# Kernel optimization log

Measured on AMD Instinct MI355X. Metric: run time of the kernel, lower is better.

## Reference

```python
import jax, jax.numpy as jnp
import numpy as np

# ---- dims (mirror reconstructed HybridSignToTextModel) ----
INPUT_SIZE = 256
CONV_CH = 512
ENC_HID = 512          # per-direction encoder GRU hidden
ENC_OUT = 2 * ENC_HID  # bidirectional concat = 1024
DEC_LAYERS = 2
DEC_HID = 512
EMB = 512
VOCAB = 8000
ATTN = 512
MAX_DEC = 50
SOS, EOS, PAD = 1, 2, 0


def _gru_cell(x, h, Wih, Whh, bih, bhh):
    # torch GRUCell math. x:(B,I) h:(B,H) Wih:(3H,I) Whh:(3H,H)
    gi = x @ Wih.T + bih
    gh = h @ Whh.T + bhh
    H = h.shape[-1]
    ir, iz, inn = gi[:, :H], gi[:, H:2*H], gi[:, 2*H:]
    hr, hz, hn = gh[:, :H], gh[:, H:2*H], gh[:, 2*H:]
    r = jax.nn.sigmoid(ir + hr)
    z = jax.nn.sigmoid(iz + hz)
    n = jnp.tanh(inn + r * hn)
    return (1.0 - z) * n + z * h


def _gru_layer(xs, h0, Wih, Whh, bih, bhh, reverse=False):
    # xs: (T,B,I) -> outputs (T,B,H), final h (B,H)
    def step(h, x):
        h = _gru_cell(x, h, Wih, Whh, bih, bhh)
        return h, h
    hT, ys = jax.lax.scan(step, h0, xs, reverse=reverse)
    return ys, hT


def _conv1d(x, w, b, stride):
    # x:(B,C,T) w:(O,C,K) 'same'-ish padding K//2
    k = w.shape[-1]
    y = jax.lax.conv_general_dilated(x, w, (stride,), [(k // 2, k // 2)],
                                     dimension_numbers=("NCH", "OIH", "NCH"))
    return y + b[None, :, None]


def setup_inputs() -> dict:
    key = jax.random.key(0)
    ks = iter(jax.random.split(key, 40))
    def rn(shape, s=0.05):
        return (jax.random.normal(next(ks), shape, dtype=jnp.float32) * s)
    p = {}
    p["features"] = jax.random.normal(next(ks), (32, 512, INPUT_SIZE), dtype=jnp.float32)
    # conv encoder: 2 conv1d layers, stride 2 each, ReLU
    p["conv_w1"] = rn((CONV_CH, INPUT_SIZE, 5)); p["conv_b1"] = rn((CONV_CH,))
    p["conv_w2"] = rn((CONV_CH, CONV_CH, 5)); p["conv_b2"] = rn((CONV_CH,))
    # bidirectional encoder GRU (1 layer)
    for d in ("f", "b"):
        p[f"enc_Wih_{d}"] = rn((3 * ENC_HID, CONV_CH))
        p[f"enc_Whh_{d}"] = rn((3 * ENC_HID, ENC_HID))
        p[f"enc_bih_{d}"] = rn((3 * ENC_HID,))
        p[f"enc_bhh_{d}"] = rn((3 * ENC_HID,))
    # hidden bridge: 2*ENC_HID -> DEC_LAYERS*DEC_HID
    p["bridge_W"] = rn((DEC_LAYERS * DEC_HID, 2 * ENC_HID)); p["bridge_b"] = rn((DEC_LAYERS * DEC_HID,))
    # decoder embedding
    p["emb"] = rn((VOCAB, EMB), 0.1)
    # Bahdanau attention
    p["attn_We"] = rn((ATTN, ENC_OUT)); p["attn_Wd"] = rn((ATTN, DEC_HID)); p["attn_v"] = rn((ATTN,))
    # decoder GRU: 2 layers; layer0 in = EMB+ENC_OUT, layer1 in = DEC_HID
    ins = [EMB + ENC_OUT, DEC_HID]
    for l in range(DEC_LAYERS):
        p[f"dec_Wih{l}"] = rn((3 * DEC_HID, ins[l]))
        p[f"dec_Whh{l}"] = rn((3 * DEC_HID, DEC_HID))
        p[f"dec_bih{l}"] = rn((3 * DEC_HID,))
        p[f"dec_bhh{l}"] = rn((3 * DEC_HID,))
    # output proj: DEC_HID + ENC_OUT -> VOCAB
    p["proj_W"] = rn((VOCAB, DEC_HID + ENC_OUT)); p["proj_b"] = rn((VOCAB,))
    return p


def reference(features, conv_w1, conv_b1, conv_w2, conv_b2,
              enc_Wih_f, enc_Whh_f, enc_bih_f, enc_bhh_f,
              enc_Wih_b, enc_Whh_b, enc_bih_b, enc_bhh_b,
              bridge_W, bridge_b, emb, attn_We, attn_Wd, attn_v,
              dec_Wih0, dec_Whh0, dec_bih0, dec_bhh0,
              dec_Wih1, dec_Whh1, dec_bih1, dec_bhh1,
              proj_W, proj_b):
    B = features.shape[0]
    # ---- conv encoder ----
    x = features.transpose(0, 2, 1)                 # (B,C,T)
    x = jax.nn.relu(_conv1d(x, conv_w1, conv_b1, 2))
    x = jax.nn.relu(_conv1d(x, conv_w2, conv_b2, 2))
    x = x.transpose(2, 0, 1)                        # (T',B,C)
    # ---- bidirectional GRU encoder ----
    h0 = jnp.zeros((B, ENC_HID), features.dtype)
    yf, hf = _gru_layer(x, h0, enc_Wih_f, enc_Whh_f, enc_bih_f, enc_bhh_f)
    yb, hb = _gru_layer(x, h0, enc_Wih_b, enc_Whh_b, enc_bih_b, enc_bhh_b, reverse=True)
    enc_out = jnp.concatenate([yf, yb], -1).transpose(1, 0, 2)   # (B,T',2H)
    combined = jnp.concatenate([hf, hb], -1)                      # (B,2H)
    dec_h = (combined @ bridge_W.T + bridge_b).reshape(B, DEC_LAYERS, DEC_HID).transpose(1, 0, 2)
    # precompute attention keys
    enc_proj = jnp.einsum("bte,ae->bta", enc_out, attn_We)       # (B,T',A)

    def attention(h_top):
        score = jnp.einsum("bta,a->bt", jnp.tanh(enc_proj + (h_top @ attn_Wd.T)[:, None, :]), attn_v)
        w = jax.nn.softmax(score, axis=-1)
        return jnp.einsum("bt,bte->be", w, enc_out)               # (B,2H)

    def decode_step(carry, _):
        tok, h = carry                                            # h: (L,B,H)
        e = emb[tok]                                              # (B,EMB)
        ctx = attention(h[-1])
        g0 = _gru_cell(jnp.concatenate([e, ctx], -1), h[0], dec_Wih0, dec_Whh0, dec_bih0, dec_bhh0)
        g1 = _gru_cell(g0, h[1], dec_Wih1, dec_Whh1, dec_bih1, dec_bhh1)
        logits = jnp.concatenate([g1, ctx], -1) @ proj_W.T + proj_b
        nxt = jnp.argmax(logits, -1)
        return (nxt, jnp.stack([g0, g1])), nxt

    init_tok = jnp.full((B,), SOS, dtype=jnp.int32)
    _, toks = jax.lax.scan(decode_step, (init_tok, dec_h), None, length=MAX_DEC - 1)
    decoded = jnp.concatenate([init_tok[:, None], toks.T], axis=1)  # (B,MAX_DEC)
    return decoded
```

## Files before the change

kernel.cpp:

```cpp
#include <hip/hip_runtime.h>
#include <math.h>

#define DINLINE __device__ __forceinline__

DINLINE float sigmoidf_(float x) { return 1.f / (1.f + expf(-x)); }

__device__ __align__(256) float g_ws[36200000];

__global__ void im2col1_kernel(const float* __restrict__ feat, float* __restrict__ P) {
  size_t i = (size_t)blockIdx.x * 256 + threadIdx.x;
  int col = (int)(i % 1280);
  int row = (int)(i / 1280);
  int c = col / 5, k = col - c * 5;
  int l = row & 255, b = row >> 8;
  int pos = 2 * l + k - 2;
  P[i] = (pos >= 0 && pos < 512) ? feat[((size_t)b * 512 + pos) * 256 + c] : 0.f;
}

__global__ void im2col2_kernel(const float* __restrict__ y1, float* __restrict__ P) {
  size_t i = (size_t)blockIdx.x * 256 + threadIdx.x;
  int col = (int)(i % 2560);
  int row = (int)(i / 2560);
  int c = col / 5, k = col - c * 5;
  int l = row & 127, b = row >> 7;
  int pos = 2 * l + k - 2;
  P[i] = (pos >= 0 && pos < 256) ? y1[((size_t)b * 256 + pos) * 512 + c] : 0.f;
}

__global__ __launch_bounds__(256) void sgemm128(
    const float* __restrict__ A, const float* __restrict__ B,
    const float* __restrict__ bias, float* __restrict__ C,
    int M, int N, int K, int relu) {
  __shared__ float As[8][132];
  __shared__ float Bs[8][132];
  int bm = blockIdx.y * 128, bn = blockIdx.x * 128;
  int tid = threadIdx.x;
  int tx = tid & 15, ty = tid >> 4;
  float acc[8][8];
#pragma unroll
  for (int i = 0; i < 8; ++i)
#pragma unroll
    for (int j = 0; j < 8; ++j) acc[i][j] = 0.f;
  int lr = tid >> 1;
  int lc = (tid & 1) * 4;
  const float* Arow = A + (size_t)(bm + lr) * K + lc;
  const float* Brow = B + (size_t)(bn + lr) * K + lc;
  for (int k0 = 0; k0 < K; k0 += 8) {
    float4 av = *(const float4*)(Arow + k0);
    float4 bv = *(const float4*)(Brow + k0);
    As[lc + 0][lr] = av.x; As[lc + 1][lr] = av.y; As[lc + 2][lr] = av.z; As[lc + 3][lr] = av.w;
    Bs[lc + 0][lr] = bv.x; Bs[lc + 1][lr] = bv.y; Bs[lc + 2][lr] = bv.z; Bs[lc + 3][lr] = bv.w;
    __syncthreads();
#pragma unroll
    for (int kk = 0; kk < 8; ++kk) {
      float4 a0 = *(const float4*)&As[kk][ty * 8];
      float4 a1 = *(const float4*)&As[kk][ty * 8 + 4];
      float4 b0 = *(const float4*)&Bs[kk][tx * 8];
      float4 b1 = *(const float4*)&Bs[kk][tx * 8 + 4];
      float aa[8] = {a0.x, a0.y, a0.z, a0.w, a1.x, a1.y, a1.z, a1.w};
      float bb[8] = {b0.x, b0.y, b0.z, b0.w, b1.x, b1.y, b1.z, b1.w};
#pragma unroll
      for (int i = 0; i < 8; ++i)
#pragma unroll
        for (int j = 0; j < 8; ++j) acc[i][j] += aa[i] * bb[j];
    }
    __syncthreads();
  }
#pragma unroll
  for (int i = 0; i < 8; ++i) {
    int m = bm + ty * 8 + i;
#pragma unroll
    for (int j = 0; j < 8; ++j) {
      int n = bn + tx * 8 + j;
      float v = acc[i][j] + (bias ? bias[n] : 0.f);
      if (relu) v = fmaxf(v, 0.f);
      C[(size_t)m * N + n] = v;
    }
  }
}

__global__ __launch_bounds__(128) void enc_gru_step(
    const float* __restrict__ gi_f, const float* __restrict__ gi_b,
    const float* __restrict__ Whh_f, const float* __restrict__ bhh_f,
    const float* __restrict__ Whh_b, const float* __restrict__ bhh_b,
    const float* __restrict__ h_in, float* __restrict__ h_out,
    float* __restrict__ enc_out, int s) {
  int dir = blockIdx.x >> 7;
  int j = ((blockIdx.x & 127) << 2) + (threadIdx.x >> 5);
  int b = threadIdx.x & 31;
  __shared__ float4 hs4[4096];
  const float4* hbase = (const float4*)(h_in + dir * 32 * 512);
  for (int i = threadIdx.x; i < 4096; i += 128) {
    int bb = i >> 7, kf = i & 127;
    hs4[(bb << 7) + (kf ^ (bb & 7))] = hbase[i];
  }
  __syncthreads();
  const float* gi = dir ? gi_b : gi_f;
  const float* Whh = dir ? Whh_b : Whh_f;
  const float* bhh = dir ? bhh_b : bhh_f;
  int t = dir ? (127 - s) : s;
  const float4* wr = (const float4*)(Whh + (size_t)j * 512);
  const float4* wz = (const float4*)(Whh + (size_t)(512 + j) * 512);
  const float4* wn = (const float4*)(Whh + (size_t)(1024 + j) * 512);
  const float4* hrow = hs4 + b * 128;
  int sw = b & 7;
  float sr = 0.f, sz = 0.f, sn = 0.f;
#pragma unroll 4
  for (int kf = 0; kf < 128; ++kf) {
    float4 hv = hrow[kf ^ sw];
    float4 r4 = wr[kf];
    float4 z4 = wz[kf];
    float4 n4 = wn[kf];
    sr += hv.x * r4.x + hv.y * r4.y + hv.z * r4.z + hv.w * r4.w;
    sz += hv.x * z4.x + hv.y * z4.y + hv.z * z4.z + hv.w * z4.w;
    sn += hv.x * n4.x + hv.y * n4.y + hv.z * n4.z + hv.w * n4.w;
  }
  const float* g = gi + ((size_t)b * 128 + t) * 1536;
  float r = sigmoidf_(g[j] + sr + bhh[j]);
  float z = sigmoidf_(g[512 + j] + sz + bhh[512 + j]);
  float n = tanhf(g[1024 + j] + r * (sn + bhh[1024 + j]));
  float4 hj4 = hrow[(j >> 2) ^ sw];
  float hj = ((const float*)&hj4)[j & 3];
  float hnew = (1.f - z) * n + z * hj;
  h_out[dir * 32 * 512 + b * 512 + j] = hnew;
  enc_out[((size_t)b * 128 + t) * 1024 + dir * 512 + j] = hnew;
}

__global__ __launch_bounds__(256) void dec_gru_fused(
    const float* __restrict__ A1, const int* __restrict__ tokidx, int len1,
    const float* __restrict__ A2, int len2,
    const float* __restrict__ Wih, const float* __restrict__ bih,
    const float* __restrict__ Whh, const float* __restrict__ bhh,
    const float* __restrict__ h_in, float* __restrict__ h_out,
    unsigned long long* __restrict__ keys_zero) {
  __shared__ float4 buf[4096];
  int tid = threadIdx.x;
  int b = tid & 31, j = (blockIdx.x << 3) + (tid >> 5);
  if (keys_zero && blockIdx.x == 0 && tid < 32) keys_zero[tid] = 0ULL;
  int Kin = len1 + len2;
  const float4* wir = (const float4*)(Wih + (size_t)j * Kin);
  const float4* wiz = (const float4*)(Wih + (size_t)(512 + j) * Kin);
  const float4* win = (const float4*)(Wih + (size_t)(1024 + j) * Kin);
  int K4 = Kin >> 2, len1_4 = len1 >> 2;
  float gr = 0.f, gz = 0.f, gn = 0.f;
  int sw5 = b & 31;
  for (int k0 = 0; k0 < K4; k0 += 32) {
    __syncthreads();
    for (int idx = tid; idx < 1024; idx += 256) {
      int bb = idx >> 5, kf = idx & 31;
      int gk = k0 + kf;
      float4 v;
      if (gk < len1_4) {
        const float* src = tokidx ? (A1 + (size_t)tokidx[bb] * len1) : (A1 + (size_t)bb * len1);
        v = ((const float4*)src)[gk];
      } else {
        v = ((const float4*)(A2 + (size_t)bb * len2))[gk - len1_4];
      }
      buf[(bb << 5) + (kf ^ (bb & 31))] = v;
    }
    __syncthreads();
    const float4* xrow = buf + (b << 5);
    const float4* wr_ = wir + k0;
    const float4* wz_ = wiz + k0;
    const float4* wn_ = win + k0;
#pragma unroll 4
    for (int kf = 0; kf < 32; ++kf) {
      float4 xv = xrow[kf ^ sw5];
      float4 r4 = wr_[kf];
      float4 z4 = wz_[kf];
      float4 n4 = wn_[kf];
      gr += xv.x * r4.x + xv.y * r4.y + xv.z * r4.z + xv.w * r4.w;
      gz += xv.x * z4.x + xv.y * z4.y + xv.z * z4.z + xv.w * z4.w;
      gn += xv.x * n4.x + xv.y * n4.y + xv.z * n4.z + xv.w * n4.w;
    }
  }
  __syncthreads();
  const float4* hbase = (const float4*)h_in;
  for (int i = tid; i < 4096; i += 256) {
    int bb = i >> 7, kf = i & 127;
    buf[(bb << 7) + (kf ^ (bb & 7))] = hbase[i];
  }
  __syncthreads();
  const float4* whr = (const float4*)(Whh + (size_t)j * 512);
  const float4* whz = (const float4*)(Whh + (size_t)(512 + j) * 512);
  const float4* whn = (const float4*)(Whh + (size_t)(1024 + j) * 512);
  const float4* hrow = buf + (b << 7);
  int sw = b & 7;
  float sr = 0.f, sz = 0.f, sn = 0.f;
#pragma unroll 4
  for (int kf = 0; kf < 128; ++kf) {
    float4 hv = hrow[kf ^ sw];
    float4 r4 = whr[kf];
    float4 z4 = whz[kf];
    float4 n4 = whn[kf];
    sr += hv.x * r4.x + hv.y * r4.y + hv.z * r4.z + hv.w * r4.w;
    sz += hv.x * z4.x + hv.y * z4.y + hv.z * z4.z + hv.w * z4.w;
    sn += hv.x * n4.x + hv.y * n4.y + hv.z * n4.z + hv.w * n4.w;
  }
  float r = sigmoidf_(gr + bih[j] + sr + bhh[j]);
  float z = sigmoidf_(gz + bih[512 + j] + sz + bhh[512 + j]);
  float n = tanhf(gn + bih[1024 + j] + r * (sn + bhh[1024 + j]));
  float4 hj4 = hrow[(j >> 2) ^ sw];
  float hj = ((const float*)&hj4)[j & 3];
  h_out[b * 512 + j] = (1.f - z) * n + z * hj;
}

__global__ __launch_bounds__(256) void gemvB(
    const float* __restrict__ A1, const int* __restrict__ tokidx, int len1,
    const float* __restrict__ A2, int len2,
    const float* __restrict__ W, const float* __restrict__ bias,
    float* __restrict__ out0, float* __restrict__ out1, int split, int N, int K) {
  int tid = threadIdx.x;
  int s = tid & 7, nl = tid >> 3;
  int n = blockIdx.x * 32 + nl;
  __shared__ float4 xs4[32 * 32];
  float acc[32];
#pragma unroll
  for (int b = 0; b < 32; ++b) acc[b] = 0.f;
  const float4* W4 = (const float4*)(W + (size_t)n * K);
  int K4 = K >> 2;
  int len1_4 = len1 >> 2;
  for (int k0 = 0; k0 < K4; k0 += 32) {
    __syncthreads();
    for (int idx = tid; idx < 1024; idx += 256) {
      int b = idx >> 5, kf = idx & 31;
      int gk = k0 + kf;
      float4 v;
      if (gk < len1_4) {
        const float* src = tokidx ? (A1 + (size_t)tokidx[b] * len1) : (A1 + (size_t)b * len1);
        v = ((const float4*)src)[gk];
      } else {
        v = ((const float4*)(A2 + (size_t)b * len2))[gk - len1_4];
      }
      xs4[idx] = v;
    }
    __syncthreads();
    const float4* wp = W4 + k0;
#pragma unroll
    for (int j = 0; j < 4; ++j) {
      float4 wv = wp[j * 8 + s];
      const float4* xp = xs4 + j * 8 + s;
#pragma unroll
      for (int b = 0; b < 32; ++b) {
        float4 xv = xp[b * 32];
        acc[b] += wv.x * xv.x + wv.y * xv.y + wv.z * xv.z + wv.w * xv.w;
      }
    }
  }
#pragma unroll
  for (int b = 0; b < 32; ++b) {
    float v = acc[b];
    v += __shfl_xor(v, 1);
    v += __shfl_xor(v, 2);
    v += __shfl_xor(v, 4);
    acc[b] = v;
  }
  if (s == 0) {
    float bv = bias ? bias[n] : 0.f;
#pragma unroll
    for (int b = 0; b < 32; ++b) {
      float val = acc[b] + bv;
      if (n < split) out0[(size_t)b * split + n] = val;
      else out1[(size_t)b * (N - split) + (n - split)] = val;
    }
  }
}

__global__ __launch_bounds__(256) void proj_argmax_kernel(
    const float* __restrict__ A1, int len1,
    const float* __restrict__ A2, int len2,
    const float* __restrict__ W, const float* __restrict__ bias,
    unsigned long long* __restrict__ keys) {
  int tid = threadIdx.x;
  int s = tid & 7, nl = tid >> 3;
  int n = blockIdx.x * 32 + nl;
  __shared__ float4 xs4[32 * 32];
  __shared__ unsigned long long ksh[32][33];
  float acc[32];
#pragma unroll
  for (int b = 0; b < 32; ++b) acc[b] = 0.f;
  int K = len1 + len2;
  const float4* W4 = (const float4*)(W + (size_t)n * K);
  int K4 = K >> 2;
  int len1_4 = len1 >> 2;
  for (int k0 = 0; k0 < K4; k0 += 32) {
    __syncthreads();
    for (int idx = tid; idx < 1024; idx += 256) {
      int b = idx >> 5, kf = idx & 31;
      int gk = k0 + kf;
      float4 v;
      if (gk < len1_4) v = ((const float4*)(A1 + (size_t)b * len1))[gk];
      else v = ((const float4*)(A2 + (size_t)b * len2))[gk - len1_4];
      xs4[idx] = v;
    }
    __syncthreads();
    const float4* wp = W4 + k0;
#pragma unroll
    for (int j = 0; j < 4; ++j) {
      float4 wv = wp[j * 8 + s];
      const float4* xp = xs4 + j * 8 + s;
#pragma unroll
      for (int b = 0; b < 32; ++b) {
        float4 xv = xp[b * 32];
        acc[b] += wv.x * xv.x + wv.y * xv.y + wv.z * xv.z + wv.w * xv.w;
      }
    }
  }
#pragma unroll
  for (int b = 0; b < 32; ++b) {
    float v = acc[b];
    v += __shfl_xor(v, 1);
    v += __shfl_xor(v, 2);
    v += __shfl_xor(v, 4);
    acc[b] = v;
  }
  if (s == 0) {
    float bv = bias[n];
#pragma unroll
    for (int b = 0; b < 32; ++b) {
      float val = acc[b] + bv;
      unsigned u = __float_as_uint(val);
      u = (u & 0x80000000u) ? ~u : (u | 0x80000000u);
      ksh[nl][b] = ((unsigned long long)u << 32) | (unsigned long long)(0xFFFFFFFFu - (unsigned)n);
    }
  }
  __syncthreads();
  if (tid < 32) {
    unsigned long long best = 0ULL;
#pragma unroll 8
    for (int q = 0; q < 32; ++q) {
      unsigned long long v = ksh[q][tid];
      if (v > best) best = v;
    }
    atomicMax(&keys[tid], best);
  }
}

__global__ __launch_bounds__(512) void attn_fused(
    const float* __restrict__ h1,
    const float* __restrict__ Wd,
    const float* __restrict__ v,
    const float* __restrict__ enc_proj,
    const float* __restrict__ enc_out,
    float* __restrict__ ctx,
    const unsigned long long* __restrict__ keys,
    int* __restrict__ tok, int* __restrict__ decoded, int step) {
  int b = blockIdx.x;
  int tid = threadIdx.x;
  if (step > 0 && b == 0 && tid < 32) {
    unsigned long long k = keys[tid];
    int n = (int)(0xFFFFFFFFu - (unsigned)(k & 0xFFFFFFFFull));
    tok[tid] = n;
    decoded[tid * 50 + step] = n;
  }
  __shared__ float hs[512];
  __shared__ float d[512];
  __shared__ float red[512];
  __shared__ float sc[128];
  hs[tid] = h1[b * 512 + tid];
  __syncthreads();
  {
    const float* w = Wd + (size_t)tid * 512;
    float s = 0.f;
    for (int k = 0; k < 512; k += 4) {
      float4 wv = *(const float4*)&w[k];
      float4 hv = *(const float4*)&hs[k];
      s += hv.x * wv.x + hv.y * wv.y + hv.z * wv.z + hv.w * wv.w;
    }
    d[tid] = s;
  }
  __syncthreads();
  {
    int t = tid >> 2, part = tid & 3;
    const float* ep = enc_proj + ((size_t)b * 128 + t) * 512 + part * 128;
    const float* dd = d + part * 128;
    const float* vv = v + part * 128;
    float s = 0.f;
    for (int a = 0; a < 128; ++a) s += tanhf(ep[a] + dd[a]) * vv[a];
    red[tid] = s;
  }
  __syncthreads();
  if (tid < 128) sc[tid] = red[tid * 4] + red[tid * 4 + 1] + red[tid * 4 + 2] + red[tid * 4 + 3];
  __syncthreads();
  if (tid == 0) {
    float m = -1e30f;
    for (int t = 0; t < 128; ++t) m = fmaxf(m, sc[t]);
    float sum = 0.f;
    for (int t = 0; t < 128; ++t) { float e = expf(sc[t] - m); sc[t] = e; sum += e; }
    float inv = 1.f / sum;
    for (int t = 0; t < 128; ++t) sc[t] *= inv;
  }
  __syncthreads();
  for (int e = tid; e < 1024; e += 512) {
    const float* eo = enc_out + (size_t)b * 131072 + e;
    float s = 0.f;
    for (int t = 0; t < 128; ++t) s += sc[t] * eo[(size_t)t * 1024];
    ctx[b * 1024 + e] = s;
  }
}

__global__ void final_tok_kernel(const unsigned long long* __restrict__ keys,
                                 int* __restrict__ decoded) {
  int b = threadIdx.x;
  if (b >= 32) return;
  int n = (int)(0xFFFFFFFFu - (unsigned)(keys[b] & 0xFFFFFFFFull));
  decoded[b * 50 + 49] = n;
}

__global__ void init_kernel(int* __restrict__ tok, int* __restrict__ decoded) {
  int b = threadIdx.x;
  if (b >= 32) return;
  tok[b] = 1;
  decoded[b * 50] = 1;
}

__global__ void zero_kernel(float* __restrict__ p, int n) {
  int i = blockIdx.x * 256 + threadIdx.x;
  if (i < n) p[i] = 0.f;
}

extern "C" void kernel_launch(void* const* d_in, const int* in_sizes, int n_in,
                              void* d_out, int out_size, void* d_ws, size_t ws_size,
                              hipStream_t stream) {
  const float* features  = (const float*)d_in[0];
  const float* conv_w1   = (const float*)d_in[1];
  const float* conv_b1   = (const float*)d_in[2];
  const float* conv_w2   = (const float*)d_in[3];
  const float* conv_b2   = (const float*)d_in[4];
  const float* enc_Wih_f = (const float*)d_in[5];
  const float* enc_Whh_f = (const float*)d_in[6];
  const float* enc_bih_f = (const float*)d_in[7];
  const float* enc_bhh_f = (const float*)d_in[8];
  const float* enc_Wih_b = (const float*)d_in[9];
  const float* enc_Whh_b = (const float*)d_in[10];
  const float* enc_bih_b = (const float*)d_in[11];
  const float* enc_bhh_b = (const float*)d_in[12];
  const float* bridge_W  = (const float*)d_in[13];
  const float* bridge_b  = (const float*)d_in[14];
  const float* emb       = (const float*)d_in[15];
  const float* attn_We   = (const float*)d_in[16];
  const float* attn_Wd   = (const float*)d_in[17];
  const float* attn_v    = (const float*)d_in[18];
  const float* dec_Wih0  = (const float*)d_in[19];
  const float* dec_Whh0  = (const float*)d_in[20];
  const float* dec_bih0  = (const float*)d_in[21];
  const float* dec_bhh0  = (const float*)d_in[22];
  const float* dec_Wih1  = (const float*)d_in[23];
  const float* dec_Whh1  = (const float*)d_in[24];
  const float* dec_bih1  = (const float*)d_in[25];
  const float* dec_bhh1  = (const float*)d_in[26];
  const float* proj_W    = (const float*)d_in[27];
  const float* proj_b    = (const float*)d_in[28];
  int* decoded = (int*)d_out;

  float* ws = nullptr;
  hipGetSymbolAddress((void**)&ws, HIP_SYMBOL(g_ws));
  float* P       = ws;
  float* y1      = ws + 10485760;
  float* x2      = ws + 14680064;
  float* gi_f    = ws + 16777216;
  float* gi_b    = ws + 23068672;
  float* enc_out = ws + 29360128;
  float* enc_pj  = ws + 33554432;
  float* h_enc   = ws + 35651584;
  float* h0d     = ws + 35717120;
  float* h1d     = ws + 35749888;
  float* ctxb    = ws + 35782656;
  unsigned long long* keys = (unsigned long long*)(ws + 35815424);
  int*   tok     = (int*)(ws + 35815488);

  im2col1_kernel<<<40960, 256, 0, stream>>>(features, P);
  sgemm128<<<dim3(4, 64), 256, 0, stream>>>(P, conv_w1, conv_b1, y1, 8192, 512, 1280, 1);
  im2col2_kernel<<<40960, 256, 0, stream>>>(y1, P);
  sgemm128<<<dim3(4, 32), 256, 0, stream>>>(P, conv_w2, conv_b2, x2, 4096, 512, 2560, 1);

  sgemm128<<<dim3(12, 32), 256, 0, stream>>>(x2, enc_Wih_f, enc_bih_f, gi_f, 4096, 1536, 512, 0);
  sgemm128<<<dim3(12, 32), 256, 0, stream>>>(x2, enc_Wih_b, enc_bih_b, gi_b, 4096, 1536, 512, 0);

  zero_kernel<<<256, 256, 0, stream>>>(h_enc, 65536);
  for (int s = 0; s < 128; ++s) {
    enc_gru_step<<<256, 128, 0, stream>>>(gi_f, gi_b,
        enc_Whh_f, enc_bhh_f, enc_Whh_b, enc_bhh_b,
        h_enc + (s & 1) * 32768, h_enc + ((s + 1) & 1) * 32768, enc_out, s);
  }
  float* h_fin = h_enc;

  gemvB<<<32, 256, 0, stream>>>(h_fin, nullptr, 512, h_fin + 16384, 512,
      bridge_W, bridge_b, h0d, h1d, 512, 1024, 1024);

  sgemm128<<<dim3(4, 32), 256, 0, stream>>>(enc_out, attn_We, nullptr, enc_pj, 4096, 512, 1024, 0);

  init_kernel<<<1, 64, 0, stream>>>(tok, decoded);

  for (int s = 0; s < 49; ++s) {
    int cur = s & 1, nxt = (s + 1) & 1;
    attn_fused<<<32, 512, 0, stream>>>(h1d + cur * 16384, attn_Wd, attn_v,
                                       enc_pj, enc_out, ctxb, keys, tok, decoded, s);
    dec_gru_fused<<<64, 256, 0, stream>>>(emb, tok, 512, ctxb, 1024,
        dec_Wih0, dec_bih0, dec_Whh0, dec_bhh0,
        h0d + cur * 16384, h0d + nxt * 16384, nullptr);
    dec_gru_fused<<<64, 256, 0, stream>>>(h0d + nxt * 16384, nullptr, 512, nullptr, 0,
        dec_Wih1, dec_bih1, dec_Whh1, dec_bhh1,
        h1d + cur * 16384, h1d + nxt * 16384, keys);
    proj_argmax_kernel<<<250, 256, 0, stream>>>(h1d + nxt * 16384, 512, ctxb, 1024,
        proj_W, proj_b, keys);
  }
  final_tok_kernel<<<1, 32, 0, stream>>>(keys, decoded);
}
```

Measured before the change: 19.93 ms.

## Replace per-step launches with persistent encoder and decoder kernels using grid barriers

The encoder GRU now runs as one persistent kernel with one block per (direction, batch). Each block keeps its hidden state in shared memory and loops over all 128 timesteps, so the 128 launches go away. The decoder's 49 steps of attention, two GRU layers and projection-argmax are fused into a single persistent 256-block kernel that synchronizes with a software global barrier, removing about 200 launches. In exchange, every encoder block rereads the full Whh matrix each step, which may make it bandwidth-bound. The spin barrier requires all 256 blocks to be co-resident and adds atomic and fence overhead at each phase.

```diff
diff --git a/kernel.cpp b/kernel.cpp
--- a/kernel.cpp
+++ b/kernel.cpp
@@ -6,6 +6,34 @@
 DINLINE float sigmoidf_(float x) { return 1.f / (1.f + expf(-x)); }
 
 __device__ __align__(256) float g_ws[36200000];
+
+__device__ unsigned g_cnt;
+__device__ unsigned g_epoch;
+
+#define GRID_BAR()                                                     \
+  do {                                                                 \
+    __syncthreads();                                                   \
+    if (threadIdx.x == 0) {                                            \
+      __threadfence();                                                 \
+      bar_target += 1u;                                                \
+      unsigned prev_ = atomicAdd(&g_cnt, 1u);                          \
+      if (prev_ == 255u) {                                             \
+        atomicExch(&g_cnt, 0u);                                        \
+        __threadfence();                                               \
+        atomicExch(&g_epoch, bar_target);                              \
+      } else {                                                         \
+        while (atomicAdd(&g_epoch, 0u) < bar_target) {                 \
+          __builtin_amdgcn_s_sleep(2);                                 \
+        }                                                              \
+      }                                                                \
+      __threadfence();                                                 \
+    }                                                                  \
+    __syncthreads();                                                   \
+  } while (0)
+
+__global__ void reset_bar_kernel() {
+  if (threadIdx.x == 0) { g_cnt = 0u; g_epoch = 0u; }
+}
 
 __global__ void im2col1_kernel(const float* __restrict__ feat, float* __restrict__ P) {
   size_t i = (size_t)blockIdx.x * 256 + threadIdx.x;
@@ -79,130 +107,54 @@
   }
 }
 
-__global__ __launch_bounds__(128) void enc_gru_step(
+__global__ __launch_bounds__(512) void enc_persist2(
     const float* __restrict__ gi_f, const float* __restrict__ gi_b,
     const float* __restrict__ Whh_f, const float* __restrict__ bhh_f,
     const float* __restrict__ Whh_b, const float* __restrict__ bhh_b,
-    const float* __restrict__ h_in, float* __restrict__ h_out,
-    float* __restrict__ enc_out, int s) {
-  int dir = blockIdx.x >> 7;
-  int j = ((blockIdx.x & 127) << 2) + (threadIdx.x >> 5);
-  int b = threadIdx.x & 31;
-  __shared__ float4 hs4[4096];
-  const float4* hbase = (const float4*)(h_in + dir * 32 * 512);
-  for (int i = threadIdx.x; i < 4096; i += 128) {
-    int bb = i >> 7, kf = i & 127;
-    hs4[(bb << 7) + (kf ^ (bb & 7))] = hbase[i];
-  }
-  __syncthreads();
-  const float* gi = dir ? gi_b : gi_f;
+    float* __restrict__ h_fin, float* __restrict__ enc_out) {
+  __shared__ float hcur[512];
+  __shared__ float gh[1536];
+  int dir = blockIdx.x >> 5;
+  int b = blockIdx.x & 31;
+  int tid = threadIdx.x;
+  int sl = tid & 7, nl = tid >> 3;
+  const float* gi  = dir ? gi_b  : gi_f;
   const float* Whh = dir ? Whh_b : Whh_f;
   const float* bhh = dir ? bhh_b : bhh_f;
-  int t = dir ? (127 - s) : s;
-  const float4* wr = (const float4*)(Whh + (size_t)j * 512);
-  const float4* wz = (const float4*)(Whh + (size_t)(512 + j) * 512);
-  const float4* wn = (const float4*)(Whh + (size_t)(1024 + j) * 512);
-  const float4* hrow = hs4 + b * 128;
-  int sw = b & 7;
-  float sr = 0.f, sz = 0.f, sn = 0.f;
+  hcur[tid] = 0.f;
+  int j = tid;
+  float bhr = bhh[j], bhz = bhh[512 + j], bhn = bhh[1024 + j];
+  __syncthreads();
+  for (int s = 0; s < 128; ++s) {
+    int t = dir ? (127 - s) : s;
 #pragma unroll 4
-  for (int kf = 0; kf < 128; ++kf) {
-    float4 hv = hrow[kf ^ sw];
-    float4 r4 = wr[kf];
-    float4 z4 = wz[kf];
-    float4 n4 = wn[kf];
-    sr += hv.x * r4.x + hv.y * r4.y + hv.z * r4.z + hv.w * r4.w;
-    sz += hv.x * z4.x + hv.y * z4.y + hv.z * z4.z + hv.w * z4.w;
-    sn += hv.x * n4.x + hv.y * n4.y + hv.z * n4.z + hv.w * n4.w;
-  }
-  const float* g = gi + ((size_t)b * 128 + t) * 1536;
-  float r = sigmoidf_(g[j] + sr + bhh[j]);
-  float z = sigmoidf_(g[512 + j] + sz + bhh[512 + j]);
-  float n = tanhf(g[1024 + j] + r * (sn + bhh[1024 + j]));
-  float4 hj4 = hrow[(j >> 2) ^ sw];
-  float hj = ((const float*)&hj4)[j & 3];
-  float hnew = (1.f - z) * n + z * hj;
-  h_out[dir * 32 * 512 + b * 512 + j] = hnew;
-  enc_out[((size_t)b * 128 + t) * 1024 + dir * 512 + j] = hnew;
-}
-
-__global__ __launch_bounds__(256) void dec_gru_fused(
-    const float* __restrict__ A1, const int* __restrict__ tokidx, int len1,
-    const float* __restrict__ A2, int len2,
-    const float* __restrict__ Wih, const float* __restrict__ bih,
-    const float* __restrict__ Whh, const float* __restrict__ bhh,
-    const float* __restrict__ h_in, float* __restrict__ h_out,
-    unsigned long long* __restrict__ keys_zero) {
-  __shared__ float4 buf[4096];
-  int tid = threadIdx.x;
-  int b = tid & 31, j = (blockIdx.x << 3) + (tid >> 5);
-  if (keys_zero && blockIdx.x == 0 && tid < 32) keys_zero[tid] = 0ULL;
-  int Kin = len1 + len2;
-  const float4* wir = (const float4*)(Wih + (size_t)j * Kin);
-  const float4* wiz = (const float4*)(Wih + (size_t)(512 + j) * Kin);
-  const float4* win = (const float4*)(Wih + (size_t)(1024 + j) * Kin);
-  int K4 = Kin >> 2, len1_4 = len1 >> 2;
-  float gr = 0.f, gz = 0.f, gn = 0.f;
-  int sw5 = b & 31;
-  for (int k0 = 0; k0 < K4; k0 += 32) {
-    __syncthreads();
-    for (int idx = tid; idx < 1024; idx += 256) {
-      int bb = idx >> 5, kf = idx & 31;
-      int gk = k0 + kf;
-      float4 v;
-      if (gk < len1_4) {
-        const float* src = tokidx ? (A1 + (size_t)tokidx[bb] * len1) : (A1 + (size_t)bb * len1);
-        v = ((const float4*)src)[gk];
-      } else {
-        v = ((const float4*)(A2 + (size_t)bb * len2))[gk - len1_4];
-      }
-      buf[(bb << 5) + (kf ^ (bb & 31))] = v;
-    }
-    __syncthreads();
-    const float4* xrow = buf + (b << 5);
-    const float4* wr_ = wir + k0;
-    const float4* wz_ = wiz + k0;
-    const float4* wn_ = win + k0;
-#pragma unroll 4
-    for (int kf = 0; kf < 32; ++kf) {
-      float4 xv = xrow[kf ^ sw5];
-      float4 r4 = wr_[kf];
-      float4 z4 = wz_[kf];
-      float4 n4 = wn_[kf];
-      gr += xv.x * r4.x + xv.y * r4.y + xv.z * r4.z + xv.w * r4.w;
-      gz += xv.x * z4.x + xv.y * z4.y + xv.z * z4.z + xv.w * z4.w;
-      gn += xv.x * n4.x + xv.y * n4.y + xv.z * n4.z + xv.w * n4.w;
-    }
-  }
-  __syncthreads();
-  const float4* hbase = (const float4*)h_in;
-  for (int i = tid; i < 4096; i += 256) {
-    int bb = i >> 7, kf = i & 127;
-    buf[(bb << 7) + (kf ^ (bb & 7))] = hbase[i];
-  }
-  __syncthreads();
-  const float4* whr = (const float4*)(Whh + (size_t)j * 512);
-  const float4* whz = (const float4*)(Whh + (size_t)(512 + j) * 512);
-  const float4* whn = (const float4*)(Whh + (size_t)(1024 + j) * 512);
-  const float4* hrow = buf + (b << 7);
-  int sw = b & 7;
-  float sr = 0.f, sz = 0.f, sn = 0.f;
-#pragma unroll 4
-  for (int kf = 0; kf < 128; ++kf) {
-    float4 hv = hrow[kf ^ sw];
-    float4 r4 = whr[kf];
-    float4 z4 = whz[kf];
-    float4 n4 = whn[kf];
-    sr += hv.x * r4.x + hv.y * r4.y + hv.z * r4.z + hv.w * r4.w;
-    sz += hv.x * z4.x + hv.y * z4.y + hv.z * z4.z + hv.w * z4.w;
-    sn += hv.x * n4.x + hv.y * n4.y + hv.z * n4.z + hv.w * n4.w;
-  }
-  float r = sigmoidf_(gr + bih[j] + sr + bhh[j]);
-  float z = sigmoidf_(gz + bih[512 + j] + sz + bhh[512 + j]);
-  float n = tanhf(gn + bih[1024 + j] + r * (sn + bhh[1024 + j]));
-  float4 hj4 = hrow[(j >> 2) ^ sw];
-  float hj = ((const float*)&hj4)[j & 3];
-  h_out[b * 512 + j] = (1.f - z) * n + z * hj;
+    for (int pass = 0; pass < 24; ++pass) {
+      int m = pass * 64 + nl;
+      const float4* wp = (const float4*)(Whh + (size_t)m * 512);
+      float a = 0.f;
+#pragma unroll
+      for (int q = 0; q < 16; ++q) {
+        float4 wv = wp[q * 8 + sl];
+        float4 hv = *(const float4*)&hcur[(q * 8 + sl) * 4];
+        a += wv.x * hv.x + wv.y * hv.y + wv.z * hv.z + wv.w * hv.w;
+      }
+      a += __shfl_xor(a, 1);
+      a += __shfl_xor(a, 2);
+      a += __shfl_xor(a, 4);
+      if (sl == 0) gh[m] = a;
+    }
+    __syncthreads();
+    const float* g = gi + ((size_t)b * 128 + t) * 1536;
+    float r = sigmoidf_(g[j] + gh[j] + bhr);
+    float z = sigmoidf_(g[512 + j] + gh[512 + j] + bhz);
+    float n = tanhf(g[1024 + j] + r * (gh[1024 + j] + bhn));
+    float hnew = (1.f - z) * n + z * hcur[j];
+    __syncthreads();
+    hcur[j] = hnew;
+    enc_out[((size_t)b * 128 + t) * 1024 + dir * 512 + j] = hnew;
+    __syncthreads();
+  }
+  h_fin[dir * 16384 + b * 512 + j] = hcur[j];
 }
 
 __global__ __launch_bounds__(256) void gemvB(
@@ -266,145 +218,265 @@
   }
 }
 
-__global__ __launch_bounds__(256) void proj_argmax_kernel(
-    const float* __restrict__ A1, int len1,
-    const float* __restrict__ A2, int len2,
-    const float* __restrict__ W, const float* __restrict__ bias,
-    unsigned long long* __restrict__ keys) {
-  int tid = threadIdx.x;
-  int s = tid & 7, nl = tid >> 3;
-  int n = blockIdx.x * 32 + nl;
-  __shared__ float4 xs4[32 * 32];
-  __shared__ unsigned long long ksh[32][33];
-  float acc[32];
-#pragma unroll
-  for (int b = 0; b < 32; ++b) acc[b] = 0.f;
-  int K = len1 + len2;
-  const float4* W4 = (const float4*)(W + (size_t)n * K);
-  int K4 = K >> 2;
-  int len1_4 = len1 >> 2;
-  for (int k0 = 0; k0 < K4; k0 += 32) {
-    __syncthreads();
-    for (int idx = tid; idx < 1024; idx += 256) {
-      int b = idx >> 5, kf = idx & 31;
-      int gk = k0 + kf;
-      float4 v;
-      if (gk < len1_4) v = ((const float4*)(A1 + (size_t)b * len1))[gk];
-      else v = ((const float4*)(A2 + (size_t)b * len2))[gk - len1_4];
-      xs4[idx] = v;
-    }
-    __syncthreads();
-    const float4* wp = W4 + k0;
-#pragma unroll
-    for (int j = 0; j < 4; ++j) {
-      float4 wv = wp[j * 8 + s];
-      const float4* xp = xs4 + j * 8 + s;
+__global__ __launch_bounds__(256) void dec_persist(
+    const float* __restrict__ emb, const float* __restrict__ attn_Wd,
+    const float* __restrict__ attn_v,
+    const float* __restrict__ enc_pj, const float* __restrict__ enc_out,
+    const float* __restrict__ dec_Wih0, const float* __restrict__ dec_bih0,
+    const float* __restrict__ dec_Whh0, const float* __restrict__ dec_bhh0,
+    const float* __restrict__ dec_Wih1, const float* __restrict__ dec_bih1,
+    const float* __restrict__ dec_Whh1, const float* __restrict__ dec_bhh1,
+    const float* __restrict__ proj_W, const float* __restrict__ proj_b,
+    float* __restrict__ h0d, float* __restrict__ h1d,
+    float* __restrict__ ctxb, float* __restrict__ dbuf,
+    unsigned long long* __restrict__ keys, int* __restrict__ tok,
+    int* __restrict__ decoded) {
+  __shared__ float4 SB[1024];
+  __shared__ unsigned long long ksh[32 * 33];
+  __shared__ float d_s[512];
+  __shared__ float red_s[256];
+  __shared__ float sc_s[128];
+  unsigned bar_target = 0u;
+  int blk = blockIdx.x, tid = threadIdx.x;
+  int s8 = tid & 7, nl = tid >> 3;
+  int bb31 = tid & 31, jj = tid >> 5;
+
+  for (int s = 0; s < 49; ++s) {
+    int cur = s & 1, nxt = (s + 1) & 1;
+    const float* h1cur = h1d + cur * 16384;
+
+    if (blk < 16) {
+      int n = blk * 32 + nl;
+      float acc[32];
+#pragma unroll
+      for (int b = 0; b < 32; ++b) acc[b] = 0.f;
+      const float4* W4 = (const float4*)(attn_Wd + (size_t)n * 512);
+      for (int k0 = 0; k0 < 128; k0 += 32) {
+        __syncthreads();
+        for (int idx = tid; idx < 1024; idx += 256) {
+          int b = idx >> 5, kf = idx & 31;
+          SB[idx] = ((const float4*)(h1cur + (size_t)b * 512))[k0 + kf];
+        }
+        __syncthreads();
+        const float4* wp = W4 + k0;
+#pragma unroll
+        for (int j = 0; j < 4; ++j) {
+          float4 wv = wp[j * 8 + s8];
+          const float4* xp = SB + j * 8 + s8;
+#pragma unroll
+          for (int b = 0; b < 32; ++b) {
+            float4 xv = xp[b * 32];
+            acc[b] += wv.x * xv.x + wv.y * xv.y + wv.z * xv.z + wv.w * xv.w;
+          }
+        }
+      }
 #pragma unroll
       for (int b = 0; b < 32; ++b) {
-        float4 xv = xp[b * 32];
-        acc[b] += wv.x * xv.x + wv.y * xv.y + wv.z * xv.z + wv.w * xv.w;
-      }
-    }
-  }
-#pragma unroll
-  for (int b = 0; b < 32; ++b) {
-    float v = acc[b];
-    v += __shfl_xor(v, 1);
-    v += __shfl_xor(v, 2);
-    v += __shfl_xor(v, 4);
-    acc[b] = v;
-  }
-  if (s == 0) {
-    float bv = bias[n];
-#pragma unroll
-    for (int b = 0; b < 32; ++b) {
-      float val = acc[b] + bv;
-      unsigned u = __float_as_uint(val);
-      u = (u & 0x80000000u) ? ~u : (u | 0x80000000u);
-      ksh[nl][b] = ((unsigned long long)u << 32) | (unsigned long long)(0xFFFFFFFFu - (unsigned)n);
-    }
-  }
-  __syncthreads();
-  if (tid < 32) {
-    unsigned long long best = 0ULL;
+        float v = acc[b];
+        v += __shfl_xor(v, 1);
+        v += __shfl_xor(v, 2);
+        v += __shfl_xor(v, 4);
+        if (s8 == 0) dbuf[(size_t)b * 512 + n] = v;
+      }
+    } else if (blk == 16 && s > 0 && tid < 32) {
+      unsigned long long k = keys[tid];
+      int n = (int)(0xFFFFFFFFu - (unsigned)(k & 0xFFFFFFFFull));
+      tok[tid] = n;
+      decoded[tid * 50 + s] = n;
+    }
+    GRID_BAR();
+
+    if (blk < 32) {
+      int b = blk;
+      d_s[tid] = dbuf[b * 512 + tid];
+      d_s[tid + 256] = dbuf[b * 512 + tid + 256];
+      __syncthreads();
+      {
+        int t = tid >> 1, part = tid & 1;
+        const float* ep = enc_pj + ((size_t)b * 128 + t) * 512 + part * 256;
+        const float* dd = d_s + part * 256;
+        const float* vv = attn_v + part * 256;
+        float sv = 0.f;
+        for (int a = 0; a < 256; ++a) sv += tanhf(ep[a] + dd[a]) * vv[a];
+        red_s[tid] = sv;
+      }
+      __syncthreads();
+      if (tid < 128) sc_s[tid] = red_s[tid * 2] + red_s[tid * 2 + 1];
+      __syncthreads();
+      if (tid == 0) {
+        float m = -1e30f;
+        for (int t = 0; t < 128; ++t) m = fmaxf(m, sc_s[t]);
+        float sum = 0.f;
+        for (int t = 0; t < 128; ++t) { float e = expf(sc_s[t] - m); sc_s[t] = e; sum += e; }
+        float inv = 1.f / sum;
+        for (int t = 0; t < 128; ++t) sc_s[t] *= inv;
+      }
+      __syncthreads();
+      for (int e = tid; e < 1024; e += 256) {
+        const float* eo = enc_out + (size_t)b * 131072 + e;
+        float sv = 0.f;
+        for (int t = 0; t < 128; ++t) sv += sc_s[t] * eo[(size_t)t * 1024];
+        ctxb[b * 1024 + e] = sv;
+      }
+    } else if (blk == 32 && tid < 32) {
+      keys[tid] = 0ULL;
+    }
+    GRID_BAR();
+
+    for (int layer = 0; layer < 2; ++layer) {
+      if (blk < 64) {
+        const float* A1   = layer ? (h0d + nxt * 16384) : emb;
+        const int* tki    = layer ? (const int*)0 : tok;
+        int len1          = 512;
+        const float* A2   = layer ? (const float*)0 : ctxb;
+        int len2          = layer ? 0 : 1024;
+        const float* Wih  = layer ? dec_Wih1 : dec_Wih0;
+        const float* bih  = layer ? dec_bih1 : dec_bih0;
+        const float* Whh  = layer ? dec_Whh1 : dec_Whh0;
+        const float* bhh  = layer ? dec_bhh1 : dec_bhh0;
+        const float* h_in = layer ? (h1d + cur * 16384) : (h0d + cur * 16384);
+        float* h_out      = layer ? (h1d + nxt * 16384) : (h0d + nxt * 16384);
+        int b = bb31, j = (blk << 3) + jj;
+        int Kin = len1 + len2;
+        int K4 = Kin >> 2, len1_4 = len1 >> 2;
+        int sw5 = b & 31;
+        const float4* wir = (const float4*)(Wih + (size_t)j * Kin);
+        const float4* wiz = (const float4*)(Wih + (size_t)(512 + j) * Kin);
+        const float4* win = (const float4*)(Wih + (size_t)(1024 + j) * Kin);
+        float gr = 0.f, gz = 0.f, gn = 0.f;
+        for (int k0 = 0; k0 < K4; k0 += 32) {
+          __syncthreads();
+          for (int idx = tid; idx < 1024; idx += 256) {
+            int bs = idx >> 5, kf = idx & 31;
+            int gk = k0 + kf;
+            float4 v;
+            if (gk < len1_4) {
+              const float* src = tki ? (A1 + (size_t)tki[bs] * len1) : (A1 + (size_t)bs * len1);
+              v = ((const float4*)src)[gk];
+            } else {
+              v = ((const float4*)(A2 + (size_t)bs * len2))[gk - len1_4];
+            }
+            SB[(bs << 5) + (kf ^ (bs & 31))] = v;
+          }
+          __syncthreads();
+          const float4* xrow = SB + (b << 5);
+          const float4* wr_ = wir + k0;
+          const float4* wz_ = wiz + k0;
+          const float4* wn_ = win + k0;
+#pragma unroll 4
+          for (int kf = 0; kf < 32; ++kf) {
+            float4 xv = xrow[kf ^ sw5];
+            float4 r4 = wr_[kf];
+            float4 z4 = wz_[kf];
+            float4 n4 = wn_[kf];
+            gr += xv.x * r4.x + xv.y * r4.y + xv.z * r4.z + xv.w * r4.w;
+            gz += xv.x * z4.x + xv.y * z4.y + xv.z * z4.z + xv.w * z4.w;
+            gn += xv.x * n4.x + xv.y * n4.y + xv.z * n4.z + xv.w * n4.w;
+          }
+        }
+        const float4* whr = (const float4*)(Whh + (size_t)j * 512);
+        const float4* whz = (const float4*)(Whh + (size_t)(512 + j) * 512);
+        const float4* whn = (const float4*)(Whh + (size_t)(1024 + j) * 512);
+        float sr = 0.f, sz = 0.f, sn = 0.f;
+        for (int k0 = 0; k0 < 128; k0 += 32) {
+          __syncthreads();
+          for (int idx = tid; idx < 1024; idx += 256) {
+            int bs = idx >> 5, kf = idx & 31;
+            float4 v = ((const float4*)(h_in + (size_t)bs * 512))[k0 + kf];
+            SB[(bs << 5) + (kf ^ (bs & 31))] = v;
+          }
+          __syncthreads();
+          const float4* xrow = SB + (b << 5);
+          const float4* wr_ = whr + k0;
+          const float4* wz_ = whz + k0;
+          const float4* wn_ = whn + k0;
+#pragma unroll 4
+          for (int kf = 0; kf < 32; ++kf) {
+            float4 xv = xrow[kf ^ sw5];
+            float4 r4 = wr_[kf];
+            float4 z4 = wz_[kf];
+            float4 n4 = wn_[kf];
+            sr += xv.x * r4.x + xv.y * r4.y + xv.z * r4.z + xv.w * r4.w;
+            sz += xv.x * z4.x + xv.y * z4.y + xv.z * z4.z + xv.w * z4.w;
+            sn += xv.x * n4.x + xv.y * n4.y + xv.z * n4.z + xv.w * n4.w;
+          }
+        }
+        float r = sigmoidf_(gr + bih[j] + sr + bhh[j]);
+        float z = sigmoidf_(gz + bih[512 + j] + sz + bhh[512 + j]);
+        float n = tanhf(gn + bih[1024 + j] + r * (sn + bhh[1024 + j]));
+        float hj = h_in[b * 512 + j];
+        h_out[b * 512 + j] = (1.f - z) * n + z * hj;
+      }
+      GRID_BAR();
+    }
+
+    if (blk < 250) {
+      const float* h1n = h1d + nxt * 16384;
+      int n = blk * 32 + nl;
+      float acc[32];
+#pragma unroll
+      for (int b = 0; b < 32; ++b) acc[b] = 0.f;
+      const float4* W4 = (const float4*)(proj_W + (size_t)n * 1536);
+      for (int k0 = 0; k0 < 384; k0 += 32) {
+        __syncthreads();
+        for (int idx = tid; idx < 1024; idx += 256) {
+          int b = idx >> 5, kf = idx & 31;
+          int gk = k0 + kf;
+          float4 v;
+          if (gk < 128) v = ((const float4*)(h1n + (size_t)b * 512))[gk];
+          else v = ((const float4*)(ctxb + (size_t)b * 1024))[gk - 128];
+          SB[idx] = v;
+        }
+        __syncthreads();
+        const float4* wp = W4 + k0;
+#pragma unroll
+        for (int j = 0; j < 4; ++j) {
+          float4 wv = wp[j * 8 + s8];
+          const float4* xp = SB + j * 8 + s8;
+#pragma unroll
+          for (int b = 0; b < 32; ++b) {
+            float4 xv = xp[b * 32];
+            acc[b] += wv.x * xv.x + wv.y * xv.y + wv.z * xv.z + wv.w * xv.w;
+          }
+        }
+      }
+#pragma unroll
+      for (int b = 0; b < 32; ++b) {
+        float v = acc[b];
+        v += __shfl_xor(v, 1);
+        v += __shfl_xor(v, 2);
+        v += __shfl_xor(v, 4);
+        acc[b] = v;
+      }
+      if (s8 == 0) {
+        float bv = proj_b[n];
+#pragma unroll
+        for (int b = 0; b < 32; ++b) {
+          float val = acc[b] + bv;
+          unsigned u = __float_as_uint(val);
+          u = (u & 0x80000000u) ? ~u : (u | 0x80000000u);
+          ksh[nl * 33 + b] =
+              ((unsigned long long)u << 32) | (unsigned long long)(0xFFFFFFFFu - (unsigned)n);
+        }
+      }
+      __syncthreads();
+      if (tid < 32) {
+        unsigned long long best = 0ULL;
 #pragma unroll 8
-    for (int q = 0; q < 32; ++q) {
-      unsigned long long v = ksh[q][tid];
-      if (v > best) best = v;
-    }
-    atomicMax(&keys[tid], best);
-  }
-}
-
-__global__ __launch_bounds__(512) void attn_fused(
-    const float* __restrict__ h1,
-    const float* __restrict__ Wd,
-    const float* __restrict__ v,
-    const float* __restrict__ enc_proj,
-    const float* __restrict__ enc_out,
-    float* __restrict__ ctx,
-    const unsigned long long* __restrict__ keys,
-    int* __restrict__ tok, int* __restrict__ decoded, int step) {
-  int b = blockIdx.x;
-  int tid = threadIdx.x;
-  if (step > 0 && b == 0 && tid < 32) {
+        for (int q = 0; q < 32; ++q) {
+          unsigned long long v = ksh[q * 33 + tid];
+          if (v > best) best = v;
+        }
+        atomicMax(&keys[tid], best);
+      }
+      __syncthreads();
+    }
+    GRID_BAR();
+  }
+  if (blk == 0 && tid < 32) {
     unsigned long long k = keys[tid];
-    int n = (int)(0xFFFFFFFFu - (unsigned)(k & 0xFFFFFFFFull));
-    tok[tid] = n;
-    decoded[tid * 50 + step] = n;
-  }
-  __shared__ float hs[512];
-  __shared__ float d[512];
-  __shared__ float red[512];
-  __shared__ float sc[128];
-  hs[tid] = h1[b * 512 + tid];
-  __syncthreads();
-  {
-    const float* w = Wd + (size_t)tid * 512;
-    float s = 0.f;
-    for (int k = 0; k < 512; k += 4) {
-      float4 wv = *(const float4*)&w[k];
-      float4 hv = *(const float4*)&hs[k];
-      s += hv.x * wv.x + hv.y * wv.y + hv.z * wv.z + hv.w * wv.w;
-    }
-    d[tid] = s;
-  }
-  __syncthreads();
-  {
-    int t = tid >> 2, part = tid & 3;
-    const float* ep = enc_proj + ((size_t)b * 128 + t) * 512 + part * 128;
-    const float* dd = d + part * 128;
-    const float* vv = v + part * 128;
-    float s = 0.f;
-    for (int a = 0; a < 128; ++a) s += tanhf(ep[a] + dd[a]) * vv[a];
-    red[tid] = s;
-  }
-  __syncthreads();
-  if (tid < 128) sc[tid] = red[tid * 4] + red[tid * 4 + 1] + red[tid * 4 + 2] + red[tid * 4 + 3];
-  __syncthreads();
-  if (tid == 0) {
-    float m = -1e30f;
-    for (int t = 0; t < 128; ++t) m = fmaxf(m, sc[t]);
-    float sum = 0.f;
-    for (int t = 0; t < 128; ++t) { float e = expf(sc[t] - m); sc[t] = e; sum += e; }
-    float inv = 1.f / sum;
-    for (int t = 0; t < 128; ++t) sc[t] *= inv;
-  }
-  __syncthreads();
-  for (int e = tid; e < 1024; e += 512) {
-    const float* eo = enc_out + (size_t)b * 131072 + e;
-    float s = 0.f;
-    for (int t = 0; t < 128; ++t) s += sc[t] * eo[(size_t)t * 1024];
-    ctx[b * 1024 + e] = s;
-  }
-}
-
-__global__ void final_tok_kernel(const unsigned long long* __restrict__ keys,
-                                 int* __restrict__ decoded) {
-  int b = threadIdx.x;
-  if (b >= 32) return;
-  int n = (int)(0xFFFFFFFFu - (unsigned)(keys[b] & 0xFFFFFFFFull));
-  decoded[b * 50 + 49] = n;
+    decoded[tid * 50 + 49] = (int)(0xFFFFFFFFu - (unsigned)(k & 0xFFFFFFFFull));
+  }
 }
 
 __global__ void init_kernel(int* __restrict__ tok, int* __restrict__ decoded) {
@@ -412,11 +484,6 @@
   if (b >= 32) return;
   tok[b] = 1;
   decoded[b * 50] = 1;
-}
-
-__global__ void zero_kernel(float* __restrict__ p, int n) {
-  int i = blockIdx.x * 256 + threadIdx.x;
-  if (i < n) p[i] = 0.f;
 }
 
 extern "C" void kernel_launch(void* const* d_in, const int* in_sizes, int n_in,
@@ -468,6 +535,7 @@
   float* ctxb    = ws + 35782656;
   unsigned long long* keys = (unsigned long long*)(ws + 35815424);
   int*   tok     = (int*)(ws + 35815488);
+  float* dbuf    = ws + 35815520;
 
   im2col1_kernel<<<40960, 256, 0, stream>>>(features, P);
   sgemm128<<<dim3(4, 64), 256, 0, stream>>>(P, conv_w1, conv_b1, y1, 8192, 512, 1280, 1);
@@ -477,33 +545,19 @@
   sgemm128<<<dim3(12, 32), 256, 0, stream>>>(x2, enc_Wih_f, enc_bih_f, gi_f, 4096, 1536, 512, 0);
   sgemm128<<<dim3(12, 32), 256, 0, stream>>>(x2, enc_Wih_b, enc_bih_b, gi_b, 4096, 1536, 512, 0);
 
-  zero_kernel<<<256, 256, 0, stream>>>(h_enc, 65536);
-  for (int s = 0; s < 128; ++s) {
-    enc_gru_step<<<256, 128, 0, stream>>>(gi_f, gi_b,
-        enc_Whh_f, enc_bhh_f, enc_Whh_b, enc_bhh_b,
-        h_enc + (s & 1) * 32768, h_enc + ((s + 1) & 1) * 32768, enc_out, s);
-  }
-  float* h_fin = h_enc;
-
-  gemvB<<<32, 256, 0, stream>>>(h_fin, nullptr, 512, h_fin + 16384, 512,
+  enc_persist2<<<64, 512, 0, stream>>>(gi_f, gi_b,
+      enc_Whh_f, enc_bhh_f, enc_Whh_b, enc_bhh_b, h_enc, enc_out);
+
+  gemvB<<<32, 256, 0, stream>>>(h_enc, nullptr, 512, h_enc + 16384, 512,
       bridge_W, bridge_b, h0d, h1d, 512, 1024, 1024);
 
   sgemm128<<<dim3(4, 32), 256, 0, stream>>>(enc_out, attn_We, nullptr, enc_pj, 4096, 512, 1024, 0);
 
   init_kernel<<<1, 64, 0, stream>>>(tok, decoded);
-
-  for (int s = 0; s < 49; ++s) {
-    int cur = s & 1, nxt = (s + 1) & 1;
-    attn_fused<<<32, 512, 0, stream>>>(h1d + cur * 16384, attn_Wd, attn_v,
-                                       enc_pj, enc_out, ctxb, keys, tok, decoded, s);
-    dec_gru_fused<<<64, 256, 0, stream>>>(emb, tok, 512, ctxb, 1024,
-        dec_Wih0, dec_bih0, dec_Whh0, dec_bhh0,
-        h0d + cur * 16384, h0d + nxt * 16384, nullptr);
-    dec_gru_fused<<<64, 256, 0, stream>>>(h0d + nxt * 16384, nullptr, 512, nullptr, 0,
-        dec_Wih1, dec_bih1, dec_Whh1, dec_bhh1,
-        h1d + cur * 16384, h1d + nxt * 16384, keys);
-    proj_argmax_kernel<<<250, 256, 0, stream>>>(h1d + nxt * 16384, 512, ctxb, 1024,
-        proj_W, proj_b, keys);
-  }
-  final_tok_kernel<<<1, 32, 0, stream>>>(keys, decoded);
-}
+  reset_bar_kernel<<<1, 64, 0, stream>>>();
+
+  dec_persist<<<256, 256, 0, stream>>>(emb, attn_Wd, attn_v, enc_pj, enc_out,
+      dec_Wih0, dec_bih0, dec_Whh0, dec_bhh0,
+      dec_Wih1, dec_bih1, dec_Whh1, dec_bhh1,
+      proj_W, proj_b, h0d, h1d, ctxb, dbuf, keys, tok, decoded);
+}
```

Measured after the change: 34.01 ms. +70.6%, slower.
